# Optimization experiments

Hardware: AMD Instinct MI355X
Metric: run time of the kernel (lower is better)

The kernel has to match this reference:

```python
import jax, jax.numpy as jnp
import numpy as np

BN_EPS = 1e-5
LRELU_SLOPE = 0.2


def setup_inputs() -> dict:
    key = jax.random.key(0)
    ks = jax.random.split(key, 5)
    B, C1, M, C2, N, C_out = 8, 256, 4096, 128, 16384, 256
    feature = jax.random.normal(ks[0], (B, C1, M), dtype=jnp.float32)
    encoder_feature = jax.random.normal(ks[1], (B, C2, N), dtype=jnp.float32)
    interp_index = jax.random.randint(ks[2], (B, N, 1), 0, M, dtype=jnp.int64)
    # ConvTranspose1d(384, 256, 1) weight has shape [in, out, 1] -> store as [in, out]
    W = jax.random.normal(ks[3], (C1 + C2, C_out), dtype=jnp.float32) * 0.05
    b = jax.random.normal(ks[4], (C_out,), dtype=jnp.float32) * 0.05
    gamma = jnp.ones((C_out,), dtype=jnp.float32)
    beta = jnp.zeros((C_out,), dtype=jnp.float32)
    return {"feature": feature, "encoder_feature": encoder_feature,
            "interp_index": interp_index, "W": W, "b": b,
            "gamma": gamma, "beta": beta}


def reference(feature, encoder_feature, interp_index, W, b, gamma, beta):
    # feature: [B, C1, M], encoder_feature: [B, C2, N], interp_index: [B, N, 1]
    idx = interp_index[..., 0]                                  # [B, N]
    # index_points on feature.permute(0,2,1) then permute back == gather along last dim
    interp_feature = jnp.take_along_axis(feature, idx[:, None, :], axis=2)  # [B, C1, N]
    x = jnp.concatenate([encoder_feature, interp_feature], axis=1)          # [B, C1+C2, N]
    # ConvTranspose1d(kernel=1): y[b,o,n] = sum_i x[b,i,n] * W[i,o] + b[o]
    y = jnp.einsum('bin,io->bon', x, W) + b[None, :, None]      # [B, C_out, N]
    # BatchNorm1d (training mode: batch stats over (B, N), biased variance)
    mean = jnp.mean(y, axis=(0, 2), keepdims=True)
    var = jnp.mean(jnp.square(y - mean), axis=(0, 2), keepdims=True)
    y = (y - mean) * jax.lax.rsqrt(var + BN_EPS)
    y = y * gamma[None, :, None] + beta[None, :, None]
    # LeakyReLU(0.2)
    return jnp.where(y > 0, y, LRELU_SLOPE * y)
```

## Files before the change

### kernel.cpp

```cpp
#include <hip/hip_runtime.h>
#include <hip/hip_bf16.h>

#define C1    256
#define C2    128
#define COUT  256
#define MM    4096
#define NN    16384
#define BB    8
#define BN_EPS 1e-5f
#define SLOPE 0.2f

typedef float  f32x4  __attribute__((ext_vector_type(4)));
typedef __bf16 bf16x8 __attribute__((ext_vector_type(8)));
typedef short  s16x8  __attribute__((ext_vector_type(8)));

static __device__ __forceinline__ unsigned short f2bf(float f) {
    unsigned int u = __builtin_bit_cast(unsigned int, f);
    unsigned int r = (u + 0x7FFFu + ((u >> 16) & 1u)) >> 16;
    return (unsigned short)r;
}

static __device__ __forceinline__ bf16x8 ld_frag(const unsigned short* p) {
    s16x8 v = *reinterpret_cast<const s16x8*>(p);
    union { s16x8 s; bf16x8 b; } cvt;
    cvt.s = v;
    return cvt.b;
}

__global__ __launch_bounds__(256) void k1_zt(const float* __restrict__ feature,
                                             const float* __restrict__ W,
                                             float* __restrict__ Zt) {
    const int mt = blockIdx.x;
    const int ot = blockIdx.y;
    const int b  = blockIdx.z;
    const int mb = mt * 64, ob = ot * 64;
    const int tid = threadIdx.x;

    __shared__ unsigned short sA[64 * 136];
    __shared__ unsigned short sB[64 * 136];

    const int wid = tid >> 6, lane = tid & 63;
    const int r = lane & 15, g = lane >> 4;
    const int wm = (wid >> 1) * 32, wo = (wid & 1) * 32;

    f32x4 acc[2][2];
#pragma unroll
    for (int i = 0; i < 2; i++)
#pragma unroll
        for (int j = 0; j < 2; j++) acc[i][j] = (f32x4){0.f, 0.f, 0.f, 0.f};

    for (int kp = 0; kp < 2; kp++) {
        const int k0 = kp * 128;
        for (int p = tid; p < 64 * 64; p += 256) {
            int m = p & 63, k = (p >> 6) * 2;
            float f0 = feature[(size_t)(b * C1 + k0 + k) * MM + mb + m];
            float f1 = feature[(size_t)(b * C1 + k0 + k + 1) * MM + mb + m];
            ushort2 u; u.x = f2bf(f0); u.y = f2bf(f1);
            *reinterpret_cast<ushort2*>(&sA[m * 136 + k]) = u;
        }
        for (int p = tid; p < 64 * 64; p += 256) {
            int o = p & 63, k = (p >> 6) * 2;
            float f0 = W[(C2 + k0 + k) * COUT + ob + o];
            float f1 = W[(C2 + k0 + k + 1) * COUT + ob + o];
            ushort2 u; u.x = f2bf(f0); u.y = f2bf(f1);
            *reinterpret_cast<ushort2*>(&sB[o * 136 + k]) = u;
        }
        __syncthreads();

#pragma unroll
        for (int ks = 0; ks < 4; ks++) {
            const int kb = ks * 32 + g * 8;
            bf16x8 a0 = ld_frag(&sA[(wm +  0 + r) * 136 + kb]);
            bf16x8 a1 = ld_frag(&sA[(wm + 16 + r) * 136 + kb]);
            bf16x8 b0 = ld_frag(&sB[(wo +  0 + r) * 136 + kb]);
            bf16x8 b1 = ld_frag(&sB[(wo + 16 + r) * 136 + kb]);
            acc[0][0] = __builtin_amdgcn_mfma_f32_16x16x32_bf16(a0, b0, acc[0][0], 0, 0, 0);
            acc[0][1] = __builtin_amdgcn_mfma_f32_16x16x32_bf16(a0, b1, acc[0][1], 0, 0, 0);
            acc[1][0] = __builtin_amdgcn_mfma_f32_16x16x32_bf16(a1, b0, acc[1][0], 0, 0, 0);
            acc[1][1] = __builtin_amdgcn_mfma_f32_16x16x32_bf16(a1, b1, acc[1][1], 0, 0, 0);
        }
        __syncthreads();
    }

#pragma unroll
    for (int fm = 0; fm < 2; fm++)
#pragma unroll
        for (int fo = 0; fo < 2; fo++)
#pragma unroll
            for (int i = 0; i < 4; i++) {
                int m = mb + wm + fm * 16 + g * 4 + i;
                int o = ob + wo + fo * 16 + r;
                Zt[((size_t)b * MM + m) * COUT + o] = acc[fm][fo][i];
            }
}

__global__ __launch_bounds__(256) void k2_main(const float* __restrict__ enc,
                                               const float* __restrict__ W,
                                               const float* __restrict__ bias,
                                               const int*   __restrict__ idx,
                                               const float* __restrict__ Zt,
                                               float* __restrict__ y,
                                               float* __restrict__ sums,
                                               float* __restrict__ sumsq) {
    const int nt = blockIdx.x;
    const int ot = blockIdx.y;
    const int b  = blockIdx.z;
    const int nb = nt * 128, ob = ot * 64;
    const int tid = threadIdx.x;

    __shared__ unsigned short sB[128 * 136];
    __shared__ unsigned short sA[64 * 136];
    __shared__ int   sIdx[128];
    __shared__ float lsum[64], lsq[64];

    if (tid < 128) sIdx[tid] = idx[b * NN + nb + tid];
    if (tid < 64) { lsum[tid] = 0.f; lsq[tid] = 0.f; }

    for (int p = tid; p < 128 * 64; p += 256) {
        int n = p & 127, k = (p >> 7) * 2;
        float f0 = enc[(size_t)(b * C2 + k) * NN + nb + n];
        float f1 = enc[(size_t)(b * C2 + k + 1) * NN + nb + n];
        ushort2 u; u.x = f2bf(f0); u.y = f2bf(f1);
        *reinterpret_cast<ushort2*>(&sB[n * 136 + k]) = u;
    }
    for (int p = tid; p < 64 * 64; p += 256) {
        int o = p & 63, k = (p >> 6) * 2;
        float f0 = W[k * COUT + ob + o];
        float f1 = W[(k + 1) * COUT + ob + o];
        ushort2 u; u.x = f2bf(f0); u.y = f2bf(f1);
        *reinterpret_cast<ushort2*>(&sA[o * 136 + k]) = u;
    }
    __syncthreads();

    const int wid = tid >> 6, lane = tid & 63;
    const int r = lane & 15, g = lane >> 4;
    const int wo = (wid >> 1) * 32;
    const int wn = (wid & 1) * 64;

    f32x4 acc[2][4];
#pragma unroll
    for (int i = 0; i < 2; i++)
#pragma unroll
        for (int j = 0; j < 4; j++) acc[i][j] = (f32x4){0.f, 0.f, 0.f, 0.f};

#pragma unroll
    for (int ks = 0; ks < 4; ks++) {
        const int kb = ks * 32 + g * 8;
        bf16x8 a0 = ld_frag(&sA[(wo +  0 + r) * 136 + kb]);
        bf16x8 a1 = ld_frag(&sA[(wo + 16 + r) * 136 + kb]);
        bf16x8 bf[4];
#pragma unroll
        for (int fn = 0; fn < 4; fn++)
            bf[fn] = ld_frag(&sB[(wn + fn * 16 + r) * 136 + kb]);
#pragma unroll
        for (int fn = 0; fn < 4; fn++) {
            acc[0][fn] = __builtin_amdgcn_mfma_f32_16x16x32_bf16(a0, bf[fn], acc[0][fn], 0, 0, 0);
            acc[1][fn] = __builtin_amdgcn_mfma_f32_16x16x32_bf16(a1, bf[fn], acc[1][fn], 0, 0, 0);
        }
    }
    __syncthreads();

    float* Zl = reinterpret_cast<float*>(sB);
    {
        const int lr = tid & 15;
        for (int row = tid >> 4; row < 128; row += 16) {
            const float4 v = reinterpret_cast<const float4*>(
                &Zt[((size_t)b * MM + sIdx[row]) * COUT + ob])[lr];
            reinterpret_cast<float4*>(&Zl[row * 68])[lr] = v;
        }
    }
    __syncthreads();

    float bi[2][4];
#pragma unroll
    for (int fo = 0; fo < 2; fo++)
#pragma unroll
        for (int i = 0; i < 4; i++)
            bi[fo][i] = bias[ob + wo + fo * 16 + g * 4 + i];

    float s_[2][4] = {{0.f,0.f,0.f,0.f},{0.f,0.f,0.f,0.f}};
    float q_[2][4] = {{0.f,0.f,0.f,0.f},{0.f,0.f,0.f,0.f}};
#pragma unroll
    for (int fo = 0; fo < 2; fo++)
#pragma unroll
        for (int fn = 0; fn < 4; fn++) {
            const int n_loc = wn + fn * 16 + r;
            const f32x4 z = *reinterpret_cast<const f32x4*>(
                &Zl[n_loc * 68 + wo + fo * 16 + g * 4]);
#pragma unroll
            for (int i = 0; i < 4; i++) {
                int o_loc = wo + fo * 16 + g * 4 + i;
                float v = acc[fo][fn][i] + z[i] + bi[fo][i];
                y[(size_t)(b * COUT + ob + o_loc) * NN + nb + n_loc] = v;
                s_[fo][i] += v;
                q_[fo][i] += v * v;
            }
        }

#pragma unroll
    for (int d = 1; d < 16; d <<= 1)
#pragma unroll
        for (int fo = 0; fo < 2; fo++)
#pragma unroll
            for (int i = 0; i < 4; i++) {
                s_[fo][i] += __shfl_xor(s_[fo][i], d);
                q_[fo][i] += __shfl_xor(q_[fo][i], d);
            }
    if (r == 0) {
#pragma unroll
        for (int fo = 0; fo < 2; fo++)
#pragma unroll
            for (int i = 0; i < 4; i++) {
                int o_loc = wo + fo * 16 + g * 4 + i;
                atomicAdd(&lsum[o_loc], s_[fo][i]);
                atomicAdd(&lsq[o_loc],  q_[fo][i]);
            }
    }
    __syncthreads();
    if (tid < 64) {
        atomicAdd(&sums [b * COUT + ob + tid], lsum[tid]);
        atomicAdd(&sumsq[b * COUT + ob + tid], lsq[tid]);
    }
}

__global__ void k3_stats(const float* __restrict__ sums,
                         const float* __restrict__ sumsq,
                         const float* __restrict__ gamma,
                         const float* __restrict__ beta,
                         float* __restrict__ ac) {
    const int o = threadIdx.x;
    float s = 0.f, q = 0.f;
#pragma unroll
    for (int b = 0; b < BB; b++) {
        s += sums [b * COUT + o];
        q += sumsq[b * COUT + o];
    }
    const float inv_cnt = 1.0f / ((float)BB * (float)NN);
    float mean = s * inv_cnt;
    float var  = q * inv_cnt - mean * mean;
    float a = gamma[o] * rsqrtf(var + BN_EPS);
    float c = beta[o] - mean * a;
    ac[o] = a;
    ac[COUT + o] = c;
}

__global__ __launch_bounds__(256) void k4_norm(float* __restrict__ y,
                                               const float* __restrict__ ac) {
    const size_t total4 = (size_t)BB * COUT * NN / 4;
    const size_t stride = (size_t)gridDim.x * 256;
    for (size_t i = (size_t)blockIdx.x * 256 + threadIdx.x; i < total4; i += stride) {
        float4 v = reinterpret_cast<float4*>(y)[i];
        int o = (int)((i * 4) >> 14) & 255;
        float a = ac[o], c = ac[COUT + o];
        float t0 = a * v.x + c; v.x = t0 > 0.f ? t0 : SLOPE * t0;
        float t1 = a * v.y + c; v.y = t1 > 0.f ? t1 : SLOPE * t1;
        float t2 = a * v.z + c; v.z = t2 > 0.f ? t2 : SLOPE * t2;
        float t3 = a * v.w + c; v.w = t3 > 0.f ? t3 : SLOPE * t3;
        reinterpret_cast<float4*>(y)[i] = v;
    }
}

extern "C" void kernel_launch(void* const* d_in, const int* in_sizes, int n_in,
                              void* d_out, int out_size, void* d_ws, size_t ws_size,
                              hipStream_t stream) {
    const float* feature = (const float*)d_in[0];
    const float* enc     = (const float*)d_in[1];
    const int*   idx     = (const int*)  d_in[2];
    const float* W       = (const float*)d_in[3];
    const float* bias    = (const float*)d_in[4];
    const float* gamma   = (const float*)d_in[5];
    const float* beta    = (const float*)d_in[6];
    float* out = (float*)d_out;

    float* sums  = (float*)d_ws;
    float* sumsq = sums + BB * COUT;
    float* ac    = sumsq + BB * COUT;
    float* Zt    = ac + 2 * COUT;

    hipMemsetAsync(sums, 0, 2 * BB * COUT * sizeof(float), stream);

    k1_zt  <<<dim3(MM / 64, COUT / 64, BB), 256, 0, stream>>>(feature, W, Zt);
    k2_main<<<dim3(NN / 128, COUT / 64, BB), 256, 0, stream>>>(enc, W, bias, idx, Zt,
                                                               out, sums, sumsq);
    k3_stats<<<1, COUT, 0, stream>>>(sums, sumsq, gamma, beta, ac);
    k4_norm<<<2048, 256, 0, stream>>>(out, ac);
}
```

Before: 348.3 us.

## Load W fragments into registers, widen bf16 packing, gather Zt via direct-to-LDS loads

k2 now builds its W MFMA fragments directly from global memory into registers, removing the sA LDS tile and one staging pass. Both kernels pack eight bf16 values per 16-byte LDS store instead of two. The Zt row gather uses global_load_lds with an XOR-swizzled 64-float row layout to avoid bank conflicts, replacing the padded register round-trip. Launch bounds add a minimum of 4 blocks per CU. The costs are more register pressure and strided per-thread W loads.

```diff
diff --git a/kernel.cpp b/kernel.cpp
--- a/kernel.cpp
+++ b/kernel.cpp
@@ -12,7 +12,10 @@
 
 typedef float  f32x4  __attribute__((ext_vector_type(4)));
 typedef __bf16 bf16x8 __attribute__((ext_vector_type(8)));
-typedef short  s16x8  __attribute__((ext_vector_type(8)));
+typedef unsigned short u16x8 __attribute__((ext_vector_type(8)));
+
+#define GLOBAL_AS __attribute__((address_space(1)))
+#define LDS_AS    __attribute__((address_space(3)))
 
 static __device__ __forceinline__ unsigned short f2bf(float f) {
     unsigned int u = __builtin_bit_cast(unsigned int, f);
@@ -21,15 +24,14 @@
 }
 
 static __device__ __forceinline__ bf16x8 ld_frag(const unsigned short* p) {
-    s16x8 v = *reinterpret_cast<const s16x8*>(p);
-    union { s16x8 s; bf16x8 b; } cvt;
-    cvt.s = v;
+    union { u16x8 s; bf16x8 b; } cvt;
+    cvt.s = *reinterpret_cast<const u16x8*>(p);
     return cvt.b;
 }
 
-__global__ __launch_bounds__(256) void k1_zt(const float* __restrict__ feature,
-                                             const float* __restrict__ W,
-                                             float* __restrict__ Zt) {
+__global__ __launch_bounds__(256, 4) void k1_zt(const float* __restrict__ feature,
+                                                const float* __restrict__ W,
+                                                float* __restrict__ Zt) {
     const int mt = blockIdx.x;
     const int ot = blockIdx.y;
     const int b  = blockIdx.z;
@@ -51,19 +53,21 @@
 
     for (int kp = 0; kp < 2; kp++) {
         const int k0 = kp * 128;
-        for (int p = tid; p < 64 * 64; p += 256) {
-            int m = p & 63, k = (p >> 6) * 2;
-            float f0 = feature[(size_t)(b * C1 + k0 + k) * MM + mb + m];
-            float f1 = feature[(size_t)(b * C1 + k0 + k + 1) * MM + mb + m];
-            ushort2 u; u.x = f2bf(f0); u.y = f2bf(f1);
-            *reinterpret_cast<ushort2*>(&sA[m * 136 + k]) = u;
-        }
-        for (int p = tid; p < 64 * 64; p += 256) {
-            int o = p & 63, k = (p >> 6) * 2;
-            float f0 = W[(C2 + k0 + k) * COUT + ob + o];
-            float f1 = W[(C2 + k0 + k + 1) * COUT + ob + o];
-            ushort2 u; u.x = f2bf(f0); u.y = f2bf(f1);
-            *reinterpret_cast<ushort2*>(&sB[o * 136 + k]) = u;
+        for (int p = tid; p < 64 * 16; p += 256) {
+            int m = p & 63, k = (p >> 6) << 3;
+            u16x8 u;
+#pragma unroll
+            for (int j = 0; j < 8; j++)
+                u[j] = f2bf(feature[(size_t)(b * C1 + k0 + k + j) * MM + mb + m]);
+            *reinterpret_cast<u16x8*>(&sA[m * 136 + k]) = u;
+        }
+        for (int p = tid; p < 64 * 16; p += 256) {
+            int o = p & 63, k = (p >> 6) << 3;
+            u16x8 u;
+#pragma unroll
+            for (int j = 0; j < 8; j++)
+                u[j] = f2bf(W[(C2 + k0 + k + j) * COUT + ob + o]);
+            *reinterpret_cast<u16x8*>(&sB[o * 136 + k]) = u;
         }
         __syncthreads();
 
@@ -94,14 +98,14 @@
             }
 }
 
-__global__ __launch_bounds__(256) void k2_main(const float* __restrict__ enc,
-                                               const float* __restrict__ W,
-                                               const float* __restrict__ bias,
-                                               const int*   __restrict__ idx,
-                                               const float* __restrict__ Zt,
-                                               float* __restrict__ y,
-                                               float* __restrict__ sums,
-                                               float* __restrict__ sumsq) {
+__global__ __launch_bounds__(256, 4) void k2_main(const float* __restrict__ enc,
+                                                  const float* __restrict__ W,
+                                                  const float* __restrict__ bias,
+                                                  const int*   __restrict__ idx,
+                                                  const float* __restrict__ Zt,
+                                                  float* __restrict__ y,
+                                                  float* __restrict__ sums,
+                                                  float* __restrict__ sumsq) {
     const int nt = blockIdx.x;
     const int ot = blockIdx.y;
     const int b  = blockIdx.z;
@@ -109,34 +113,38 @@
     const int tid = threadIdx.x;
 
     __shared__ unsigned short sB[128 * 136];
-    __shared__ unsigned short sA[64 * 136];
-    __shared__ int   sIdx[128];
     __shared__ float lsum[64], lsq[64];
 
-    if (tid < 128) sIdx[tid] = idx[b * NN + nb + tid];
     if (tid < 64) { lsum[tid] = 0.f; lsq[tid] = 0.f; }
-
-    for (int p = tid; p < 128 * 64; p += 256) {
-        int n = p & 127, k = (p >> 7) * 2;
-        float f0 = enc[(size_t)(b * C2 + k) * NN + nb + n];
-        float f1 = enc[(size_t)(b * C2 + k + 1) * NN + nb + n];
-        ushort2 u; u.x = f2bf(f0); u.y = f2bf(f1);
-        *reinterpret_cast<ushort2*>(&sB[n * 136 + k]) = u;
-    }
-    for (int p = tid; p < 64 * 64; p += 256) {
-        int o = p & 63, k = (p >> 6) * 2;
-        float f0 = W[k * COUT + ob + o];
-        float f1 = W[(k + 1) * COUT + ob + o];
-        ushort2 u; u.x = f2bf(f0); u.y = f2bf(f1);
-        *reinterpret_cast<ushort2*>(&sA[o * 136 + k]) = u;
-    }
-    __syncthreads();
 
     const int wid = tid >> 6, lane = tid & 63;
     const int r = lane & 15, g = lane >> 4;
     const int wo = (wid >> 1) * 32;
     const int wn = (wid & 1) * 64;
 
+    bf16x8 wf[4][2];
+#pragma unroll
+    for (int ks = 0; ks < 4; ks++)
+#pragma unroll
+        for (int fr = 0; fr < 2; fr++) {
+            u16x8 tmp;
+#pragma unroll
+            for (int j = 0; j < 8; j++)
+                tmp[j] = f2bf(W[(ks * 32 + g * 8 + j) * COUT + ob + wo + fr * 16 + r]);
+            union { u16x8 u; bf16x8 b; } cv; cv.u = tmp;
+            wf[ks][fr] = cv.b;
+        }
+
+    for (int p = tid; p < 128 * 16; p += 256) {
+        int n = p & 127, k = (p >> 7) << 3;
+        u16x8 u;
+#pragma unroll
+        for (int j = 0; j < 8; j++)
+            u[j] = f2bf(enc[(size_t)(b * C2 + k + j) * NN + nb + n]);
+        *reinterpret_cast<u16x8*>(&sB[n * 136 + k]) = u;
+    }
+    __syncthreads();
+
     f32x4 acc[2][4];
 #pragma unroll
     for (int i = 0; i < 2; i++)
@@ -146,27 +154,33 @@
 #pragma unroll
     for (int ks = 0; ks < 4; ks++) {
         const int kb = ks * 32 + g * 8;
-        bf16x8 a0 = ld_frag(&sA[(wo +  0 + r) * 136 + kb]);
-        bf16x8 a1 = ld_frag(&sA[(wo + 16 + r) * 136 + kb]);
-        bf16x8 bf[4];
+        bf16x8 bfr[4];
 #pragma unroll
         for (int fn = 0; fn < 4; fn++)
-            bf[fn] = ld_frag(&sB[(wn + fn * 16 + r) * 136 + kb]);
+            bfr[fn] = ld_frag(&sB[(wn + fn * 16 + r) * 136 + kb]);
 #pragma unroll
         for (int fn = 0; fn < 4; fn++) {
-            acc[0][fn] = __builtin_amdgcn_mfma_f32_16x16x32_bf16(a0, bf[fn], acc[0][fn], 0, 0, 0);
-            acc[1][fn] = __builtin_amdgcn_mfma_f32_16x16x32_bf16(a1, bf[fn], acc[1][fn], 0, 0, 0);
+            acc[0][fn] = __builtin_amdgcn_mfma_f32_16x16x32_bf16(wf[ks][0], bfr[fn], acc[0][fn], 0, 0, 0);
+            acc[1][fn] = __builtin_amdgcn_mfma_f32_16x16x32_bf16(wf[ks][1], bfr[fn], acc[1][fn], 0, 0, 0);
         }
     }
     __syncthreads();
 
     float* Zl = reinterpret_cast<float*>(sB);
     {
-        const int lr = tid & 15;
-        for (int row = tid >> 4; row < 128; row += 16) {
-            const float4 v = reinterpret_cast<const float4*>(
-                &Zt[((size_t)b * MM + sIdx[row]) * COUT + ob])[lr];
-            reinterpret_cast<float4*>(&Zl[row * 68])[lr] = v;
+        const int lrow = lane >> 4;
+        const int lcol = lane & 15;
+        const int* idxb = idx + b * NN + nb;
+#pragma unroll
+        for (int it = 0; it < 8; it++) {
+            const int wrow = wid * 32 + it * 4;
+            const int row  = wrow + lrow;
+            const int zi   = idxb[row];
+            const float* src = &Zt[((size_t)b * MM + zi) * COUT + ob +
+                                   ((lcol ^ (row & 15)) << 2)];
+            __builtin_amdgcn_global_load_lds(
+                (const GLOBAL_AS unsigned int*)src,
+                (LDS_AS unsigned int*)(&Zl[wrow * 64]), 16, 0, 0);
         }
     }
     __syncthreads();
@@ -185,8 +199,9 @@
 #pragma unroll
         for (int fn = 0; fn < 4; fn++) {
             const int n_loc = wn + fn * 16 + r;
+            const int o4 = (wo >> 2) + fo * 4 + g;
             const f32x4 z = *reinterpret_cast<const f32x4*>(
-                &Zl[n_loc * 68 + wo + fo * 16 + g * 4]);
+                &Zl[n_loc * 64 + ((o4 ^ r) << 2)]);
 #pragma unroll
             for (int i = 0; i < 4; i++) {
                 int o_loc = wo + fo * 16 + g * 4 + i;
```

Result: faster. 325.3 us (-6.6%).
